# Optimization experiments

Measured on AMD Instinct MI355X. Metric: run time of the kernel, lower is better.

Reference implementation:

```python
import jax, jax.numpy as jnp
import numpy as np

NEG_SLOPE = 0.2  # PyG GATConv default


def gat_conv(x, src, dst, W, a_src, a_dst, bias, n):
    # x: [N, Fin] -> h: [N, Fout]
    h = x @ W
    alpha_s = h @ a_src  # [N]
    alpha_d = h @ a_dst  # [N]
    e = jax.nn.leaky_relu(alpha_s[src] + alpha_d[dst], NEG_SLOPE)  # [E]
    # segment softmax over incoming edges of each target node
    m = jax.ops.segment_max(e, dst, num_segments=n)
    e = jnp.exp(e - m[dst])
    denom = jax.ops.segment_sum(e, dst, num_segments=n)
    alpha = e / denom[dst]
    out = jax.ops.segment_sum(alpha[:, None] * h[src], dst, num_segments=n)
    return out + bias


def setup_inputs() -> dict:
    key = jax.random.key(0)
    ks = jax.random.split(key, 10)
    N, E, FIN, HID, FOUT = 100000, 3200000, 128, 32, 64
    x = jax.random.normal(ks[0], (N, FIN), dtype=jnp.float32)
    edge_index = jax.random.randint(ks[1], (2, E), 0, N, dtype=jnp.int64)
    s = 1.0 / np.sqrt(FIN)
    W1 = jax.random.normal(ks[2], (FIN, HID), dtype=jnp.float32) * s
    a1_src = jax.random.normal(ks[3], (HID,), dtype=jnp.float32) * 0.1
    a1_dst = jax.random.normal(ks[4], (HID,), dtype=jnp.float32) * 0.1
    b1 = jnp.zeros((HID,), dtype=jnp.float32)
    W2 = jax.random.normal(ks[5], (HID, FOUT), dtype=jnp.float32) * (1.0 / np.sqrt(HID))
    a2_src = jax.random.normal(ks[6], (FOUT,), dtype=jnp.float32) * 0.1
    a2_dst = jax.random.normal(ks[7], (FOUT,), dtype=jnp.float32) * 0.1
    b2 = jnp.zeros((FOUT,), dtype=jnp.float32)
    return {"x": x, "edge_index": edge_index, "W1": W1, "a1_src": a1_src,
            "a1_dst": a1_dst, "b1": b1, "W2": W2, "a2_src": a2_src,
            "a2_dst": a2_dst, "b2": b2}


def reference(x, edge_index, W1, a1_src, a1_dst, b1, W2, a2_src, a2_dst, b2):
    n = x.shape[0]
    # add self loops (GATConv default add_self_loops=True)
    loop = jnp.arange(n, dtype=edge_index.dtype)
    src = jnp.concatenate([edge_index[0], loop])
    dst = jnp.concatenate([edge_index[1], loop])
    h = gat_conv(x, src, dst, W1, a1_src, a1_dst, b1, n)
    h = jax.nn.relu(h)
    out = gat_conv(h, src, dst, W2, a2_src, a2_dst, b2, n)
    return out
```

## Files before the change

### kernel.cpp

```cpp
#include <hip/hip_runtime.h>
#include <cstdint>
#include <cmath>

#define NEG_SLOPE 0.2f
#define BSH 6
#define CSH 9
#define CBN 512
#define RATIO 8
#define PCHUNK 8192

__device__ __forceinline__ float leaky(float v) { return v > 0.f ? v : NEG_SLOPE * v; }
__device__ __forceinline__ float uf(unsigned u) { return __uint_as_float(u); }

__device__ __forceinline__ unsigned short f2bf(float f) {
    unsigned u = __float_as_uint(f);
    unsigned r = ((u >> 16) & 1u) + 0x7fffu;
    return (unsigned short)((u + r) >> 16);
}
__device__ __forceinline__ float bflo(unsigned q) { return __uint_as_float(q << 16); }
__device__ __forceinline__ float bfhi(unsigned q) { return __uint_as_float(q & 0xffff0000u); }

template <int FIN, int FOUT, int CPR, int LCPR>
__global__ __launch_bounds__(256, 4) void gemm_rows(
    const float* __restrict__ X, const float* __restrict__ W,
    const float* __restrict__ a_src, const float* __restrict__ a_dst,
    unsigned short* __restrict__ H, float* __restrict__ As, float* __restrict__ Ad,
    float* __restrict__ bmax, int N)
{
    constexpr int ROWS = 256 / CPR;
    constexpr int XST = FIN + 4;
    static_assert((1 << LCPR) == CPR && CPR * 4 == FOUT, "geometry");

    __shared__ float Ws[FIN * FOUT];
    __shared__ float Xs[ROWS * XST];
    __shared__ float wmax[4];

    const int tid = threadIdx.x;
    const int base = blockIdx.x * ROWS;

    for (int i = tid; i < FIN * FOUT / 4; i += 256)
        reinterpret_cast<float4*>(Ws)[i] = reinterpret_cast<const float4*>(W)[i];

    for (int i = tid; i < ROWS * FIN / 4; i += 256) {
        int row = i / (FIN / 4);
        int k4 = (i - row * (FIN / 4)) * 4;
        float4 v = make_float4(0.f, 0.f, 0.f, 0.f);
        if (base + row < N)
            v = *reinterpret_cast<const float4*>(&X[(size_t)(base + row) * FIN + k4]);
        *reinterpret_cast<float4*>(&Xs[row * XST + k4]) = v;
    }
    __syncthreads();

    const int colg = tid & (CPR - 1);
    const int row = tid >> LCPR;
    const int c0 = colg * 4;

    float4 acc = make_float4(0.f, 0.f, 0.f, 0.f);

#pragma unroll 2
    for (int k = 0; k < FIN; k += 4) {
        float4 xv = *reinterpret_cast<const float4*>(&Xs[row * XST + k]);
        float4 w0 = *reinterpret_cast<const float4*>(&Ws[(k + 0) * FOUT + c0]);
        float4 w1 = *reinterpret_cast<const float4*>(&Ws[(k + 1) * FOUT + c0]);
        float4 w2 = *reinterpret_cast<const float4*>(&Ws[(k + 2) * FOUT + c0]);
        float4 w3 = *reinterpret_cast<const float4*>(&Ws[(k + 3) * FOUT + c0]);
        acc.x = fmaf(xv.w, w3.x, fmaf(xv.z, w2.x, fmaf(xv.y, w1.x, fmaf(xv.x, w0.x, acc.x))));
        acc.y = fmaf(xv.w, w3.y, fmaf(xv.z, w2.y, fmaf(xv.y, w1.y, fmaf(xv.x, w0.y, acc.y))));
        acc.z = fmaf(xv.w, w3.z, fmaf(xv.z, w2.z, fmaf(xv.y, w1.z, fmaf(xv.x, w0.z, acc.z))));
        acc.w = fmaf(xv.w, w3.w, fmaf(xv.z, w2.w, fmaf(xv.y, w1.w, fmaf(xv.x, w0.w, acc.w))));
    }

    const int grow = base + row;
    if (grow < N) {
        ushort4 hv;
        hv.x = f2bf(acc.x); hv.y = f2bf(acc.y);
        hv.z = f2bf(acc.z); hv.w = f2bf(acc.w);
        *reinterpret_cast<ushort4*>(&H[(size_t)grow * FOUT + c0]) = hv;
    }

    float4 asv = *reinterpret_cast<const float4*>(&a_src[c0]);
    float4 adv = *reinterpret_cast<const float4*>(&a_dst[c0]);
    float ps = acc.x * asv.x + acc.y * asv.y + acc.z * asv.z + acc.w * asv.w;
    float pd = acc.x * adv.x + acc.y * adv.y + acc.z * adv.z + acc.w * adv.w;
#pragma unroll
    for (int ofs = 1; ofs < CPR; ofs <<= 1) {
        ps += __shfl_xor(ps, ofs);
        pd += __shfl_xor(pd, ofs);
    }
    if (colg == 0 && grow < N) { As[grow] = ps; Ad[grow] = pd; }

    float pm = (grow < N) ? ps : -3.0e38f;
#pragma unroll
    for (int ofs = 1; ofs < 64; ofs <<= 1) pm = fmaxf(pm, __shfl_xor(pm, ofs));
    if ((tid & 63) == 0) wmax[tid >> 6] = pm;
    __syncthreads();
    if (tid == 0)
        bmax[blockIdx.x] = fmaxf(fmaxf(wmax[0], wmax[1]), fmaxf(wmax[2], wmax[3]));
}

__global__ __launch_bounds__(256) void reduce_max_kernel(
    const float* __restrict__ bmax, int nb, float* __restrict__ gmax)
{
    __shared__ float sd[256];
    const int t = threadIdx.x;
    float m = -3.0e38f;
    for (int i = t; i < nb; i += 256) m = fmaxf(m, bmax[i]);
    sd[t] = m; __syncthreads();
    for (int ofs = 128; ofs; ofs >>= 1) {
        if (t < ofs) sd[t] = fmaxf(sd[t], sd[t + ofs]);
        __syncthreads();
    }
    if (t == 0) *gmax = sd[0];
}

__global__ __launch_bounds__(64) void w2prep(
    const float* __restrict__ W2, const float* __restrict__ a2s,
    const float* __restrict__ a2d, float* __restrict__ w2s, float* __restrict__ w2d)
{
    const int t = threadIdx.x;
    const int i = t & 31;
    const float* a = (t < 32) ? a2s : a2d;
    float s = 0.f;
    for (int j = 0; j < 64; ++j) s = fmaf(W2[i * 64 + j], a[j], s);
    if (t < 32) w2s[i] = s; else w2d[i] = s;
}

__global__ __launch_bounds__(256) void alpha2_kernel(
    const float* __restrict__ h1f, const float* __restrict__ w2s,
    const float* __restrict__ w2d, float* __restrict__ As2, float* __restrict__ Ad2,
    float* __restrict__ bmaxa, int N)
{
    __shared__ float wmax[4];
    const int tid = threadIdx.x;
    const int n = blockIdx.x * 256 + tid;
    float ps = 0.f, pd = 0.f;
    if (n < N) {
        const float4* p = reinterpret_cast<const float4*>(h1f + (size_t)n * 32);
#pragma unroll
        for (int w = 0; w < 8; ++w) {
            float4 v = p[w];
            ps = fmaf(v.x, w2s[4 * w + 0], ps); ps = fmaf(v.y, w2s[4 * w + 1], ps);
            ps = fmaf(v.z, w2s[4 * w + 2], ps); ps = fmaf(v.w, w2s[4 * w + 3], ps);
            pd = fmaf(v.x, w2d[4 * w + 0], pd); pd = fmaf(v.y, w2d[4 * w + 1], pd);
            pd = fmaf(v.z, w2d[4 * w + 2], pd); pd = fmaf(v.w, w2d[4 * w + 3], pd);
        }
        As2[n] = ps; Ad2[n] = pd;
    }
    float pm = (n < N) ? ps : -3.0e38f;
#pragma unroll
    for (int ofs = 1; ofs < 64; ofs <<= 1) pm = fmaxf(pm, __shfl_xor(pm, ofs));
    if ((tid & 63) == 0) wmax[tid >> 6] = pm;
    __syncthreads();
    if (tid == 0)
        bmaxa[blockIdx.x] = fmaxf(fmaxf(wmax[0], wmax[1]), fmaxf(wmax[2], wmax[3]));
}

__global__ __launch_bounds__(256) void chunk_hist(
    const int* __restrict__ dst, int* __restrict__ pcT,
    int E, int NB, int NCC, int NCH)
{
    __shared__ int hc[2048];
    const int t = threadIdx.x;
    for (int i = t; i < 2048; i += 256) hc[i] = 0;
    __syncthreads();
    const int base = blockIdx.x * PCHUNK;
    const int end = (base + PCHUNK < E) ? base + PCHUNK : E;
    for (int e = base + t; e < end; e += 256)
        atomicAdd(&hc[dst[e] >> BSH], 1);
    __syncthreads();
    if (t < NCC) {
        int f0 = t * RATIO;
        int s = 0;
#pragma unroll
        for (int j = 0; j < RATIO; ++j) {
            int fb = f0 + j;
            if (fb < NB) s += hc[fb];
        }
        pcT[(size_t)t * NCH + blockIdx.x] = s;
    }
}

__global__ __launch_bounds__(256) void coarse_total(
    const int* __restrict__ pcT, int* __restrict__ totals, int NCH)
{
    __shared__ int sd[256];
    const int t = threadIdx.x;
    int s = 0;
    for (int i = t; i < NCH; i += 256)
        s += pcT[(size_t)blockIdx.x * NCH + i];
    sd[t] = s; __syncthreads();
    for (int ofs = 128; ofs; ofs >>= 1) {
        if (t < ofs) sd[t] += sd[t + ofs];
        __syncthreads();
    }
    if (t == 0) totals[blockIdx.x] = sd[0];
}

__global__ __launch_bounds__(256) void boffc_scan(
    const int* __restrict__ totals, int* __restrict__ boffC, int NCC)
{
    __shared__ int sd[256];
    const int t = threadIdx.x;
    int v = (t < NCC) ? totals[t] : 0;
    sd[t] = v; __syncthreads();
    for (int ofs = 1; ofs < 256; ofs <<= 1) {
        int tmp = (t >= ofs) ? sd[t - ofs] : 0;
        __syncthreads();
        sd[t] += tmp;
        __syncthreads();
    }
    if (t < NCC) boffC[t] = sd[t] - v;
    if (t == 255) boffC[NCC] = sd[255];
}

__global__ __launch_bounds__(256) void coarse_scan(
    const int* __restrict__ pcT, const int* __restrict__ boffC,
    int* __restrict__ co, int NCH)
{
    __shared__ int sd[256];
    const int c = blockIdx.x;
    const int t = threadIdx.x;
    const int base = boffC[c];
    int carry = 0;
    for (int start = 0; start < NCH; start += 256) {
        int idx = start + t;
        int v = (idx < NCH) ? pcT[(size_t)c * NCH + idx] : 0;
        sd[t] = v; __syncthreads();
        for (int ofs = 1; ofs < 256; ofs <<= 1) {
            int tmp = (t >= ofs) ? sd[t - ofs] : 0;
            __syncthreads();
            sd[t] += tmp;
            __syncthreads();
        }
        int incl = sd[t];
        int total = sd[255];
        if (idx < NCH) co[(size_t)idx * 256 + c] = base + carry + incl - v;
        carry += total;
        __syncthreads();
    }
}

__global__ __launch_bounds__(256) void coarse_partition(
    const int* __restrict__ src, const int* __restrict__ dst,
    const int* __restrict__ co, int* __restrict__ csrA, int E, int NCC)
{
    __shared__ int lcur[256], gpos[256];
    const int t = threadIdx.x;
    lcur[t] = 0;
    if (t < NCC) gpos[t] = co[(size_t)blockIdx.x * 256 + t];
    __syncthreads();
    const int base = blockIdx.x * PCHUNK;
    int bb[32], pp[32];
#pragma unroll
    for (int i = 0; i < 32; ++i) {
        int e = base + i * 256 + t;
        bb[i] = -1;
        if (e < E) {
            int sv = src[e], dv = dst[e];
            bb[i] = dv >> CSH;
            pp[i] = (sv << CSH) | (dv & (CBN - 1));
        }
    }
#pragma unroll
    for (int i = 0; i < 32; ++i) {
        if (bb[i] >= 0) {
            int b = bb[i];
            csrA[gpos[b] + atomicAdd(&lcur[b], 1)] = pp[i];
        }
    }
}

__global__ __launch_bounds__(256) void node_sort(
    const int* __restrict__ csrA, const int* __restrict__ boffC,
    int* __restrict__ off, int* __restrict__ csr, int N, int NCC, int E)
{
    __shared__ int cnt[CBN];
    __shared__ int pref[CBN];
    __shared__ int sd[256];
    const int c = blockIdx.x;
    const int t = threadIdx.x;
    const int p0 = boffC[c];
    const int p1 = boffC[c + 1];
    const int n0 = c << CSH;

    for (int i = t; i < CBN; i += 256) cnt[i] = 0;
    __syncthreads();
    for (int i = p0 + t; i < p1; i += 256)
        atomicAdd(&cnt[csrA[i] & (CBN - 1)], 1);
    __syncthreads();
    int a0 = cnt[2 * t], a1 = cnt[2 * t + 1];
    int pairsum = a0 + a1;
    sd[t] = pairsum; __syncthreads();
    for (int ofs = 1; ofs < 256; ofs <<= 1) {
        int tmp = (t >= ofs) ? sd[t - ofs] : 0;
        __syncthreads();
        sd[t] += tmp;
        __syncthreads();
    }
    int run = sd[t] - pairsum;
    pref[2 * t] = run;
    pref[2 * t + 1] = run + a0;
    int n = n0 + 2 * t;
    if (n < N) off[n] = p0 + run;
    if (n + 1 < N) off[n + 1] = p0 + run + a0;
    if (c == NCC - 1 && t == 0) off[N] = E;
    __syncthreads();
    for (int i = t; i < CBN; i += 256) cnt[i] = 0;
    __syncthreads();
    for (int i = p0 + t; i < p1; i += 256) {
        int v = csrA[i];
        int ln = v & (CBN - 1);
        int p = atomicAdd(&cnt[ln], 1);
        csr[p0 + pref[ln] + p] = v >> CSH;
    }
}

__global__ __launch_bounds__(256) void gat_agg1(
    const int* __restrict__ csr, const int* __restrict__ off,
    const float* __restrict__ As, const float* __restrict__ Ad,
    const unsigned short* __restrict__ Hb, const float* __restrict__ bias,
    const float* __restrict__ gmax, unsigned short* __restrict__ Out,
    float* __restrict__ OutF, int N)
{
    constexpr int LPR = 8;
    constexpr int EPI = 8;
    constexpr unsigned RB = 64;

    __shared__ uint2 pr[4][64];
    const int wave = threadIdx.x >> 6;
    const int lane = threadIdx.x & 63;
    const int n = blockIdx.x * 4 + wave;
    if (n >= N) return;

    const int o0 = off[n];
    const int deg = off[n + 1] - o0;
    const float adn = Ad[n];
    const float eself = leaky(As[n] + adn);
    const float m = leaky(*gmax + adn);

    uint2* myp = pr[wave];
    const char* Hc = (const char*)Hb;
    const int subg = lane / LPR;
    const unsigned f8 = (unsigned)(lane & (LPR - 1)) * 8u;

    float4 acc = make_float4(0.f, 0.f, 0.f, 0.f);
    float denp = 0.f;

    for (int c = 0; c < deg; c += 64) {
        int i = c + lane;
        float w = 0.f; unsigned sb = 0;
        if (i < deg) {
            int s = csr[o0 + i];
            w = __expf(leaky(As[s] + adn) - m);
            sb = (unsigned)s * RB;
            denp += w;
        }
        myp[lane] = make_uint2(sb, __float_as_uint(w));
        int lim = (deg - c < 64) ? deg - c : 64;
        int j = subg;
        for (; j + 3 * EPI < lim; j += 4 * EPI) {
            uint2 p0 = myp[j], p1 = myp[j + EPI], p2 = myp[j + 2 * EPI], p3 = myp[j + 3 * EPI];
            uint2 q0 = *(const uint2*)(Hc + p0.x + f8);
            uint2 q1 = *(const uint2*)(Hc + p1.x + f8);
            uint2 q2 = *(const uint2*)(Hc + p2.x + f8);
            uint2 q3 = *(const uint2*)(Hc + p3.x + f8);
            float w0 = uf(p0.y), w1 = uf(p1.y), w2 = uf(p2.y), w3 = uf(p3.y);
            acc.x = fmaf(w0, bflo(q0.x), acc.x); acc.y = fmaf(w0, bfhi(q0.x), acc.y);
            acc.z = fmaf(w0, bflo(q0.y), acc.z); acc.w = fmaf(w0, bfhi(q0.y), acc.w);
            acc.x = fmaf(w1, bflo(q1.x), acc.x); acc.y = fmaf(w1, bfhi(q1.x), acc.y);
            acc.z = fmaf(w1, bflo(q1.y), acc.z); acc.w = fmaf(w1, bfhi(q1.y), acc.w);
            acc.x = fmaf(w2, bflo(q2.x), acc.x); acc.y = fmaf(w2, bfhi(q2.x), acc.y);
            acc.z = fmaf(w2, bflo(q2.y), acc.z); acc.w = fmaf(w2, bfhi(q2.y), acc.w);
            acc.x = fmaf(w3, bflo(q3.x), acc.x); acc.y = fmaf(w3, bfhi(q3.x), acc.y);
            acc.z = fmaf(w3, bflo(q3.y), acc.z); acc.w = fmaf(w3, bfhi(q3.y), acc.w);
        }
        for (; j < lim; j += EPI) {
            uint2 p = myp[j];
            uint2 q = *(const uint2*)(Hc + p.x + f8);
            float w0 = uf(p.y);
            acc.x = fmaf(w0, bflo(q.x), acc.x); acc.y = fmaf(w0, bfhi(q.x), acc.y);
            acc.z = fmaf(w0, bflo(q.y), acc.z); acc.w = fmaf(w0, bfhi(q.y), acc.w);
        }
    }

#pragma unroll
    for (int ofs = 32; ofs >= LPR; ofs >>= 1) {
        acc.x += __shfl_xor(acc.x, ofs);
        acc.y += __shfl_xor(acc.y, ofs);
        acc.z += __shfl_xor(acc.z, ofs);
        acc.w += __shfl_xor(acc.w, ofs);
    }
#pragma unroll
    for (int ofs = 1; ofs < 64; ofs <<= 1) denp += __shfl_xor(denp, ofs);

    float wsf = __expf(eself - m);
    uint2 qs = *(const uint2*)(Hc + (size_t)n * RB + f8);
    acc.x = fmaf(wsf, bflo(qs.x), acc.x); acc.y = fmaf(wsf, bfhi(qs.x), acc.y);
    acc.z = fmaf(wsf, bflo(qs.y), acc.z); acc.w = fmaf(wsf, bfhi(qs.y), acc.w);
    float den = denp + wsf;

    if (subg == 0) {
        int fi = (lane & (LPR - 1)) * 4;
        float4 bv = *reinterpret_cast<const float4*>(&bias[fi]);
        float vx = fmaxf(acc.x / den + bv.x, 0.f);
        float vy = fmaxf(acc.y / den + bv.y, 0.f);
        float vz = fmaxf(acc.z / den + bv.z, 0.f);
        float vw = fmaxf(acc.w / den + bv.w, 0.f);
        ushort4 hv;
        hv.x = f2bf(vx); hv.y = f2bf(vy); hv.z = f2bf(vz); hv.w = f2bf(vw);
        *reinterpret_cast<ushort4*>(&Out[(size_t)n * 32 + fi]) = hv;
        *reinterpret_cast<float4*>(&OutF[(size_t)n * 32 + fi]) =
            make_float4(vx, vy, vz, vw);
    }
}

__global__ __launch_bounds__(256) void gat_agg2(
    const int* __restrict__ csr, const int* __restrict__ off,
    const float* __restrict__ As, const float* __restrict__ Ad,
    const unsigned short* __restrict__ Hb, const float* __restrict__ W2,
    const float* __restrict__ b2, const float* __restrict__ gmax,
    float* __restrict__ Out, int N)
{
    constexpr int LPR = 8;
    constexpr int EPI = 8;
    constexpr unsigned RB = 64;

    __shared__ float Ws2[32 * 64];
    __shared__ uint2 pr[4][64];
    __shared__ float aggv[4][32];

    const int tid = threadIdx.x;
    for (int i = tid; i < 32 * 64 / 4; i += 256)
        reinterpret_cast<float4*>(Ws2)[i] = reinterpret_cast<const float4*>(W2)[i];
    __syncthreads();

    const int wave = tid >> 6;
    const int lane = tid & 63;
    const int n = blockIdx.x * 4 + wave;
    if (n >= N) return;

    const int o0 = off[n];
    const int deg = off[n + 1] - o0;
    const float adn = Ad[n];
    const float eself = leaky(As[n] + adn);
    const float m = leaky(*gmax + adn);

    uint2* myp = pr[wave];
    const char* Hc = (const char*)Hb;
    const int subg = lane / LPR;
    const unsigned f8 = (unsigned)(lane & (LPR - 1)) * 8u;

    float4 acc = make_float4(0.f, 0.f, 0.f, 0.f);
    float denp = 0.f;

    for (int c = 0; c < deg; c += 64) {
        int i = c + lane;
        float w = 0.f; unsigned sb = 0;
        if (i < deg) {
            int s = csr[o0 + i];
            w = __expf(leaky(As[s] + adn) - m);
            sb = (unsigned)s * RB;
            denp += w;
        }
        myp[lane] = make_uint2(sb, __float_as_uint(w));
        int lim = (deg - c < 64) ? deg - c : 64;
        int j = subg;
        for (; j + 3 * EPI < lim; j += 4 * EPI) {
            uint2 p0 = myp[j], p1 = myp[j + EPI], p2 = myp[j + 2 * EPI], p3 = myp[j + 3 * EPI];
            uint2 q0 = *(const uint2*)(Hc + p0.x + f8);
            uint2 q1 = *(const uint2*)(Hc + p1.x + f8);
            uint2 q2 = *(const uint2*)(Hc + p2.x + f8);
            uint2 q3 = *(const uint2*)(Hc + p3.x + f8);
            float w0 = uf(p0.y), w1 = uf(p1.y), w2 = uf(p2.y), w3 = uf(p3.y);
            acc.x = fmaf(w0, bflo(q0.x), acc.x); acc.y = fmaf(w0, bfhi(q0.x), acc.y);
            acc.z = fmaf(w0, bflo(q0.y), acc.z); acc.w = fmaf(w0, bfhi(q0.y), acc.w);
            acc.x = fmaf(w1, bflo(q1.x), acc.x); acc.y = fmaf(w1, bfhi(q1.x), acc.y);
            acc.z = fmaf(w1, bflo(q1.y), acc.z); acc.w = fmaf(w1, bfhi(q1.y), acc.w);
            acc.x = fmaf(w2, bflo(q2.x), acc.x); acc.y = fmaf(w2, bfhi(q2.x), acc.y);
            acc.z = fmaf(w2, bflo(q2.y), acc.z); acc.w = fmaf(w2, bfhi(q2.y), acc.w);
            acc.x = fmaf(w3, bflo(q3.x), acc.x); acc.y = fmaf(w3, bfhi(q3.x), acc.y);
            acc.z = fmaf(w3, bflo(q3.y), acc.z); acc.w = fmaf(w3, bfhi(q3.y), acc.w);
        }
        for (; j < lim; j += EPI) {
            uint2 p = myp[j];
            uint2 q = *(const uint2*)(Hc + p.x + f8);
            float w0 = uf(p.y);
            acc.x = fmaf(w0, bflo(q.x), acc.x); acc.y = fmaf(w0, bfhi(q.x), acc.y);
            acc.z = fmaf(w0, bflo(q.y), acc.z); acc.w = fmaf(w0, bfhi(q.y), acc.w);
        }
    }

#pragma unroll
    for (int ofs = 32; ofs >= LPR; ofs >>= 1) {
        acc.x += __shfl_xor(acc.x, ofs);
        acc.y += __shfl_xor(acc.y, ofs);
        acc.z += __shfl_xor(acc.z, ofs);
        acc.w += __shfl_xor(acc.w, ofs);
    }
#pragma unroll
    for (int ofs = 1; ofs < 64; ofs <<= 1) denp += __shfl_xor(denp, ofs);

    float wsf = __expf(eself - m);
    uint2 qs = *(const uint2*)(Hc + (size_t)n * RB + f8);
    acc.x = fmaf(wsf, bflo(qs.x), acc.x); acc.y = fmaf(wsf, bfhi(qs.x), acc.y);
    acc.z = fmaf(wsf, bflo(qs.y), acc.z); acc.w = fmaf(wsf, bfhi(qs.y), acc.w);
    float den = denp + wsf;

    if (subg == 0)
        *reinterpret_cast<float4*>(&aggv[wave][(lane & (LPR - 1)) * 4]) = acc;

    float s = 0.f;
#pragma unroll
    for (int k = 0; k < 32; ++k)
        s = fmaf(aggv[wave][k], Ws2[k * 64 + lane], s);
    Out[(size_t)n * 64 + lane] = s / den + b2[lane];
}

extern "C" void kernel_launch(void* const* d_in, const int* in_sizes, int n_in,
                              void* d_out, int out_size, void* d_ws, size_t ws_size,
                              hipStream_t stream)
{
    const float* x   = (const float*)d_in[0];
    const int*   ei  = (const int*)d_in[1];
    const float* W1  = (const float*)d_in[2];
    const float* a1s = (const float*)d_in[3];
    const float* a1d = (const float*)d_in[4];
    const float* b1  = (const float*)d_in[5];
    const float* W2  = (const float*)d_in[6];
    const float* a2s = (const float*)d_in[7];
    const float* a2d = (const float*)d_in[8];
    const float* b2  = (const float*)d_in[9];

    const int N = in_sizes[0] / 128;
    const int E = in_sizes[1] / 2;
    const int NB = (N + 63) >> BSH;
    const int NCC = (N + CBN - 1) >> CSH;
    const int NCH = (E + PCHUNK - 1) / PCHUNK;
    const int* src = ei;
    const int* dst = ei + E;
    float* out = (float*)d_out;

    const int g1 = (N + 31) / 32;
    const int ga = (N + 255) / 256;

    float* ws = (float*)d_ws;
    size_t o = 0;
    unsigned short* h1b = (unsigned short*)(ws + o); o += (size_t)N * 16;
    unsigned short* h1a = (unsigned short*)(ws + o); o += (size_t)N * 16;
    float* h1f = ws + o; o += (size_t)N * 32;
    float* as1 = ws + o; o += N;
    float* ad1 = ws + o; o += N;
    float* as2 = ws + o; o += N;
    float* ad2 = ws + o; o += N;
    float* bmax = ws + o; o += (size_t)g1;
    float* bmaxa = ws + o; o += (size_t)ga;
    float* gmax1 = ws + o; o += 1;
    float* gmax2 = ws + o; o += 1;
    float* w2s = ws + o; o += 32;
    float* w2d = ws + o; o += 32;
    int* ip = (int*)(ws + o);
    size_t io = 0;
    int* pcT    = ip + io; io += (size_t)NCC * NCH;
    int* totals = ip + io; io += NCC;
    int* boffC  = ip + io; io += (NCC + 1);
    int* co     = ip + io; io += (size_t)NCH * 256;
    int* off    = ip + io; io += (N + 1);
    int* csrA   = ip + io; io += E;
    int* csr    = ip + io; io += E;

    chunk_hist<<<NCH, 256, 0, stream>>>(dst, pcT, E, NB, NCC, NCH);
    coarse_total<<<NCC, 256, 0, stream>>>(pcT, totals, NCH);
    boffc_scan<<<1, 256, 0, stream>>>(totals, boffC, NCC);
    coarse_scan<<<NCC, 256, 0, stream>>>(pcT, boffC, co, NCH);
    coarse_partition<<<NCH, 256, 0, stream>>>(src, dst, co, csrA, E, NCC);
    node_sort<<<NCC, 256, 0, stream>>>(csrA, boffC, off, csr, N, NCC, E);

    const int gn = (N + 3) / 4;

    gemm_rows<128, 32, 8, 3><<<g1, 256, 0, stream>>>(
        x, W1, a1s, a1d, h1b, as1, ad1, bmax, N);
    reduce_max_kernel<<<1, 256, 0, stream>>>(bmax, g1, gmax1);
    gat_agg1<<<gn, 256, 0, stream>>>(
        csr, off, as1, ad1, h1b, b1, gmax1, h1a, h1f, N);

    w2prep<<<1, 64, 0, stream>>>(W2, a2s, a2d, w2s, w2d);
    alpha2_kernel<<<ga, 256, 0, stream>>>(h1f, w2s, w2d, as2, ad2, bmaxa, N);
    reduce_max_kernel<<<1, 256, 0, stream>>>(bmaxa, ga, gmax2);
    gat_agg2<<<gn, 256, 0, stream>>>(
        csr, off, as2, ad2, h1a, W2, b2, gmax2, out, N);
}
```

Before: 257.0 us.

## Fuse layer-2 attention logits into layer-1 aggregation and merge small prep kernels

Layer-2 attention scores (As2/Ad2) and the per-wave max are now computed in the epilogue of gat_agg1 through a shuffle reduction, so the fp32 h1f intermediate and the separate alpha2 kernel are no longer needed. The w2prep step is folded into the first global-max reduction kernel, which removes launches. gat_agg2 stops staging W2 into shared memory and reads it straight from global memory through the cache. The cost is a larger per-node max buffer (one entry per wave) for the final reduction, plus possible global-load latency in the agg2 matvec.

Measured after the change: 316.8 us. 23.3% more time.

```diff
diff --git a/kernel.cpp b/kernel.cpp
--- a/kernel.cpp
+++ b/kernel.cpp
@@ -113,46 +113,28 @@
     if (t == 0) *gmax = sd[0];
 }
 
-__global__ __launch_bounds__(64) void w2prep(
+__global__ __launch_bounds__(256) void rmax_w2prep(
+    const float* __restrict__ bmax, int nb, float* __restrict__ gmax,
     const float* __restrict__ W2, const float* __restrict__ a2s,
     const float* __restrict__ a2d, float* __restrict__ w2s, float* __restrict__ w2d)
 {
-    const int t = threadIdx.x;
-    const int i = t & 31;
-    const float* a = (t < 32) ? a2s : a2d;
-    float s = 0.f;
-    for (int j = 0; j < 64; ++j) s = fmaf(W2[i * 64 + j], a[j], s);
-    if (t < 32) w2s[i] = s; else w2d[i] = s;
-}
-
-__global__ __launch_bounds__(256) void alpha2_kernel(
-    const float* __restrict__ h1f, const float* __restrict__ w2s,
-    const float* __restrict__ w2d, float* __restrict__ As2, float* __restrict__ Ad2,
-    float* __restrict__ bmaxa, int N)
-{
-    __shared__ float wmax[4];
-    const int tid = threadIdx.x;
-    const int n = blockIdx.x * 256 + tid;
-    float ps = 0.f, pd = 0.f;
-    if (n < N) {
-        const float4* p = reinterpret_cast<const float4*>(h1f + (size_t)n * 32);
-#pragma unroll
-        for (int w = 0; w < 8; ++w) {
-            float4 v = p[w];
-            ps = fmaf(v.x, w2s[4 * w + 0], ps); ps = fmaf(v.y, w2s[4 * w + 1], ps);
-            ps = fmaf(v.z, w2s[4 * w + 2], ps); ps = fmaf(v.w, w2s[4 * w + 3], ps);
-            pd = fmaf(v.x, w2d[4 * w + 0], pd); pd = fmaf(v.y, w2d[4 * w + 1], pd);
-            pd = fmaf(v.z, w2d[4 * w + 2], pd); pd = fmaf(v.w, w2d[4 * w + 3], pd);
-        }
-        As2[n] = ps; Ad2[n] = pd;
-    }
-    float pm = (n < N) ? ps : -3.0e38f;
-#pragma unroll
-    for (int ofs = 1; ofs < 64; ofs <<= 1) pm = fmaxf(pm, __shfl_xor(pm, ofs));
-    if ((tid & 63) == 0) wmax[tid >> 6] = pm;
-    __syncthreads();
-    if (tid == 0)
-        bmaxa[blockIdx.x] = fmaxf(fmaxf(wmax[0], wmax[1]), fmaxf(wmax[2], wmax[3]));
+    __shared__ float sd[256];
+    const int t = threadIdx.x;
+    float m = -3.0e38f;
+    for (int i = t; i < nb; i += 256) m = fmaxf(m, bmax[i]);
+    sd[t] = m; __syncthreads();
+    for (int ofs = 128; ofs; ofs >>= 1) {
+        if (t < ofs) sd[t] = fmaxf(sd[t], sd[t + ofs]);
+        __syncthreads();
+    }
+    if (t == 0) *gmax = sd[0];
+    if (t < 64) {
+        int i = t & 31;
+        const float* a = (t < 32) ? a2s : a2d;
+        float s = 0.f;
+        for (int j = 0; j < 64; ++j) s = fmaf(W2[i * 64 + j], a[j], s);
+        if (t < 32) w2s[i] = s; else w2d[i] = s;
+    }
 }
 
 __global__ __launch_bounds__(256) void chunk_hist(
@@ -319,8 +301,10 @@
     const int* __restrict__ csr, const int* __restrict__ off,
     const float* __restrict__ As, const float* __restrict__ Ad,
     const unsigned short* __restrict__ Hb, const float* __restrict__ bias,
-    const float* __restrict__ gmax, unsigned short* __restrict__ Out,
-    float* __restrict__ OutF, int N)
+    const float* __restrict__ gmax, const float* __restrict__ w2s,
+    const float* __restrict__ w2d, unsigned short* __restrict__ Out,
+    float* __restrict__ As2, float* __restrict__ Ad2,
+    float* __restrict__ bmaxw, int N)
 {
     constexpr int LPR = 8;
     constexpr int EPI = 8;
@@ -330,7 +314,10 @@
     const int wave = threadIdx.x >> 6;
     const int lane = threadIdx.x & 63;
     const int n = blockIdx.x * 4 + wave;
-    if (n >= N) return;
+    if (n >= N) {
+        if (lane == 0) bmaxw[blockIdx.x * 4 + wave] = -3.0e38f;
+        return;
+    }
 
     const int o0 = off[n];
     const int deg = off[n + 1] - o0;
@@ -399,18 +386,29 @@
     acc.z = fmaf(wsf, bflo(qs.y), acc.z); acc.w = fmaf(wsf, bfhi(qs.y), acc.w);
     float den = denp + wsf;
 
+    const int fi = (lane & (LPR - 1)) * 4;
+    float4 bv = *reinterpret_cast<const float4*>(&bias[fi]);
+    float vx = fmaxf(acc.x / den + bv.x, 0.f);
+    float vy = fmaxf(acc.y / den + bv.y, 0.f);
+    float vz = fmaxf(acc.z / den + bv.z, 0.f);
+    float vw = fmaxf(acc.w / den + bv.w, 0.f);
+
     if (subg == 0) {
-        int fi = (lane & (LPR - 1)) * 4;
-        float4 bv = *reinterpret_cast<const float4*>(&bias[fi]);
-        float vx = fmaxf(acc.x / den + bv.x, 0.f);
-        float vy = fmaxf(acc.y / den + bv.y, 0.f);
-        float vz = fmaxf(acc.z / den + bv.z, 0.f);
-        float vw = fmaxf(acc.w / den + bv.w, 0.f);
         ushort4 hv;
         hv.x = f2bf(vx); hv.y = f2bf(vy); hv.z = f2bf(vz); hv.w = f2bf(vw);
         *reinterpret_cast<ushort4*>(&Out[(size_t)n * 32 + fi]) = hv;
-        *reinterpret_cast<float4*>(&OutF[(size_t)n * 32 + fi]) =
-            make_float4(vx, vy, vz, vw);
+    }
+
+    float ps = vx * w2s[fi] + vy * w2s[fi + 1] + vz * w2s[fi + 2] + vw * w2s[fi + 3];
+    float pd = vx * w2d[fi] + vy * w2d[fi + 1] + vz * w2d[fi + 2] + vw * w2d[fi + 3];
+#pragma unroll
+    for (int ofs = 1; ofs < LPR; ofs <<= 1) {
+        ps += __shfl_xor(ps, ofs);
+        pd += __shfl_xor(pd, ofs);
+    }
+    if (lane == 0) {
+        As2[n] = ps; Ad2[n] = pd;
+        bmaxw[blockIdx.x * 4 + wave] = ps;
     }
 }
 
@@ -425,15 +423,10 @@
     constexpr int EPI = 8;
     constexpr unsigned RB = 64;
 
-    __shared__ float Ws2[32 * 64];
     __shared__ uint2 pr[4][64];
     __shared__ float aggv[4][32];
 
     const int tid = threadIdx.x;
-    for (int i = tid; i < 32 * 64 / 4; i += 256)
-        reinterpret_cast<float4*>(Ws2)[i] = reinterpret_cast<const float4*>(W2)[i];
-    __syncthreads();
-
     const int wave = tid >> 6;
     const int lane = tid & 63;
     const int n = blockIdx.x * 4 + wave;
@@ -512,7 +505,7 @@
     float s = 0.f;
 #pragma unroll
     for (int k = 0; k < 32; ++k)
-        s = fmaf(aggv[wave][k], Ws2[k * 64 + lane], s);
+        s = fmaf(aggv[wave][k], W2[k * 64 + lane], s);
     Out[(size_t)n * 64 + lane] = s / den + b2[lane];
 }
 
@@ -541,19 +534,18 @@
     float* out = (float*)d_out;
 
     const int g1 = (N + 31) / 32;
-    const int ga = (N + 255) / 256;
+    const int gn = (N + 3) / 4;
 
     float* ws = (float*)d_ws;
     size_t o = 0;
     unsigned short* h1b = (unsigned short*)(ws + o); o += (size_t)N * 16;
     unsigned short* h1a = (unsigned short*)(ws + o); o += (size_t)N * 16;
-    float* h1f = ws + o; o += (size_t)N * 32;
     float* as1 = ws + o; o += N;
     float* ad1 = ws + o; o += N;
     float* as2 = ws + o; o += N;
     float* ad2 = ws + o; o += N;
     float* bmax = ws + o; o += (size_t)g1;
-    float* bmaxa = ws + o; o += (size_t)ga;
+    float* bmaxw = ws + o; o += (size_t)gn * 4;
     float* gmax1 = ws + o; o += 1;
     float* gmax2 = ws + o; o += 1;
     float* w2s = ws + o; o += 32;
@@ -575,17 +567,13 @@
     coarse_partition<<<NCH, 256, 0, stream>>>(src, dst, co, csrA, E, NCC);
     node_sort<<<NCC, 256, 0, stream>>>(csrA, boffC, off, csr, N, NCC, E);
 
-    const int gn = (N + 3) / 4;
-
     gemm_rows<128, 32, 8, 3><<<g1, 256, 0, stream>>>(
         x, W1, a1s, a1d, h1b, as1, ad1, bmax, N);
-    reduce_max_kernel<<<1, 256, 0, stream>>>(bmax, g1, gmax1);
+    rmax_w2prep<<<1, 256, 0, stream>>>(bmax, g1, gmax1, W2, a2s, a2d, w2s, w2d);
     gat_agg1<<<gn, 256, 0, stream>>>(
-        csr, off, as1, ad1, h1b, b1, gmax1, h1a, h1f, N);
-
-    w2prep<<<1, 64, 0, stream>>>(W2, a2s, a2d, w2s, w2d);
-    alpha2_kernel<<<ga, 256, 0, stream>>>(h1f, w2s, w2d, as2, ad2, bmaxa, N);
-    reduce_max_kernel<<<1, 256, 0, stream>>>(bmaxa, ga, gmax2);
+        csr, off, as1, ad1, h1b, b1, gmax1, w2s, w2d, h1a, as2, ad2, bmaxw, N);
+
+    reduce_max_kernel<<<1, 256, 0, stream>>>(bmaxw, gn * 4, gmax2);
     gat_agg2<<<gn, 256, 0, stream>>>(
         csr, off, as2, ad2, h1a, W2, b2, gmax2, out, N);
 }
```
